# Kernel tuning notes

Measured on AMD Instinct MI355X. Metric: run time of the kernel, lower is better.

## Reference

```python
import jax, jax.numpy as jnp
import numpy as np

BLOCK = 32            # MX block size (base-class default)
FMT_MAX = 1.984375    # MXINT8 element max = 127/64 (concrete _quantize_elements choice)
QSTEP = 64.0          # quantization grid step 2^-6
BUDGET = 8.0          # cfg.msd_cycle_budget
THRESH = 0.0          # cfg.msd_budget_dynamic_threshold
ALPHA = 1.0           # cfg.msd_budget_dynamic_scale (mode='linear')
NEG = -60.0           # log2 sentinel for zero/negative values


def _safe_log2(x):
    return jnp.where(x > 0, jnp.log2(jnp.maximum(x, 1e-45)), NEG)


def _quantize_blocks(t):
    """Per-block shared fp32 scale + MXINT8-style element quantization.
    t: (rows, feat) with feat % BLOCK == 0 -> q (rows, nb, bs), scales (rows, nb)."""
    rows = t.shape[0]
    blocks = t.reshape(rows, -1, BLOCK)
    max_abs = jnp.max(jnp.abs(blocks), axis=-1)
    scales = jnp.maximum(max_abs / FMT_MAX, 1e-30)
    q = jnp.round(blocks / scales[..., None] * QSTEP) / QSTEP
    return q, scales


def _msd_truncate(value, num_digits):
    """Truncate each element to its num_digits most-significant NAF (BSD) digits."""
    abs_v = jnp.abs(value)
    sign = jnp.sign(value)
    mask = (num_digits > 0) & (abs_v > 0)
    msb_pos = jnp.floor(jnp.log2(jnp.maximum(abs_v, 1e-45)))
    scale_up = jnp.exp2(23.0 - msb_pos)              # place MSB at bit 23
    x_scaled = jnp.round(abs_v * scale_up).astype(jnp.int32)
    x_h = x_scaled >> 1
    s = x_scaled + x_h
    naf_pos = s & ~x_h
    naf_neg = x_h & ~s
    combined = naf_pos | naf_neg
    naf_width = jnp.where(
        combined > 0,
        jnp.floor(jnp.log2(jnp.maximum(combined.astype(jnp.float32), 1.0))).astype(jnp.int32) + 1,
        jnp.zeros_like(combined),
    )
    drop = jnp.clip(naf_width - num_digits.astype(jnp.int32), 0, 31)
    keep_mask = ~((jnp.int32(1) << drop) - 1)
    recon = ((naf_pos & keep_mask).astype(jnp.float32)
             - (naf_neg & keep_mask).astype(jnp.float32)) / scale_up
    return jnp.where(mask, sign * recon, jnp.zeros_like(recon))


def _forward(x, weight, bias):
    x_q, x_scales = _quantize_blocks(x)        # (N, nb, bs), (N, nb)
    w_q, w_scales = _quantize_blocks(weight)   # (O, nb, bs), (O, nb)
    # inter-block delays from shared scales
    combined_e = jnp.floor(_safe_log2(x_scales)[:, None, :]
                           + _safe_log2(w_scales)[None, :, :])   # (N, O, nb)
    e_max = jnp.max(combined_e, axis=-1)                         # (N, O)
    inter = e_max[..., None] - combined_e                        # (N, O, nb)
    # intra-block delays from activation element exponents
    abs_q = jnp.abs(x_q)
    elem_e = jnp.where(abs_q > 0, jnp.floor(jnp.log2(jnp.maximum(abs_q, 1e-45))), NEG)
    intra = jnp.max(elem_e, axis=-1, keepdims=True) - elem_e     # (N, nb, bs)
    # hybrid Glocal per-channel cycle budgets (linear dynamic mode)
    b_final = BUDGET + ALPHA * jnp.clip(e_max - THRESH, 0.0)     # (N, O)
    eff = (b_final[:, :, None, None]
           - inter[..., None]
           - intra[:, None, :, :])                               # (N, O, nb, bs)
    prod = x_q[:, None, :, :] * w_q[None, :, :, :]               # (N, O, nb, bs)
    trunc = jax.lax.stop_gradient(_msd_truncate(prod, eff))      # torch.no_grad()
    block_dot = jnp.sum(trunc, axis=-1)                          # (N, O, nb)
    out = jnp.einsum('nb,ob,nob->no', x_scales, w_scales, block_dot)
    return out + bias[None, :]


def setup_inputs() -> dict:
    key = jax.random.key(0)
    k1, k2, k3 = jax.random.split(key, 3)
    N, IN, OUT = 128, 1024, 512
    x = jax.random.normal(k1, (N, IN), dtype=jnp.float32)
    weight = jax.random.normal(k2, (OUT, IN), dtype=jnp.float32) * 0.02
    bias = jax.random.normal(k3, (OUT,), dtype=jnp.float32)
    return {"x": x, "weight": weight, "bias": bias}


def reference(x, weight, bias):
    return _forward(x, weight, bias)
```

## Files before the change

kernel.cpp:

```cpp
#include <hip/hip_runtime.h>
#include <math.h>

#define NROWS 128
#define KDIM  1024
#define ODIM  512
#define NB    32
#define BS    32

__device__ __forceinline__ int clz32(unsigned x) { return x ? __builtin_clz(x) : 32; }

__device__ __forceinline__ int naf_keep(int P, int isum, int allones) {
  int kept, h, t, c, dr;
  asm volatile(
      "v_ashrrev_i32 %1, 1, %5\n\t"
      "v_add_u32     %2, %5, %1\n\t"
      "v_xor_b32     %3, %2, %1\n\t"
      "v_ffbh_u32    %3, %3\n\t"
      "v_sub_u32     %4, %6, %3\n\t"
      "v_med3_i32    %4, %4, 0, 31\n\t"
      "v_lshlrev_b32 %3, %4, %7\n\t"
      "v_and_b32     %2, %2, %3\n\t"
      "v_and_b32     %1, %1, %3\n\t"
      "v_sub_u32     %0, %2, %1"
      : "=v"(kept), "=&v"(h), "=&v"(t), "=&v"(c), "=&v"(dr)
      : "v"(P), "v"(isum), "v"(allones));
  return kept;
}

__global__ __launch_bounds__(64)
void prep_kernel(const float* __restrict__ x, const float* __restrict__ wgt,
                 unsigned short* __restrict__ xp, unsigned char* __restrict__ wq,
                 float* __restrict__ xs, float* __restrict__ lxs,
                 float* __restrict__ wsc, float* __restrict__ lws) {
  __shared__ float sl[2112];
  const int b = blockIdx.x;
  const int lane = threadIdx.x;
  const bool isx = b < 64;
  const float* src = isx ? (x + (size_t)b * 2048)
                         : (wgt + (size_t)(b - 64) * 2048);
#pragma unroll
  for (int j = 0; j < 8; ++j) {
    float4 f = ((const float4*)src)[j * 64 + lane];
    int f0 = (j * 64 + lane) * 4;
    int s0 = f0 + (f0 >> 5);
    sl[s0] = f.x; sl[s0 + 1] = f.y; sl[s0 + 2] = f.z; sl[s0 + 3] = f.w;
  }
  __syncthreads();

  float v[32];
  float m = 0.f;
#pragma unroll
  for (int k = 0; k < 32; ++k) {
    v[k] = sl[lane * 33 + k];
    m = fmaxf(m, fabsf(v[k]));
  }
  const float scale = fmaxf(m / 1.984375f, 1e-30f);
  const int gt = (isx ? b : (b - 64)) * 64 + lane;
  const int row = gt >> 5, blk = gt & 31;

  if (isx) {
    int q[32], e[32], emax = -60;
#pragma unroll
    for (int i = 0; i < 32; ++i) {
      float t = v[i] / scale * 64.0f;
      int qi = (int)rintf(t);
      q[i] = qi;
      int a = qi < 0 ? -qi : qi;
      int ei = a ? (31 - clz32((unsigned)a)) - 6 : -60;
      e[i] = ei;
      emax = ei > emax ? ei : emax;
    }
    unsigned short u[32];
#pragma unroll
    for (int i = 0; i < 32; ++i)
      u[i] = (unsigned short)(((emax - e[i]) << 8) | (q[i] & 0xFF));
    uint4* dst = (uint4*)(xp + (size_t)row * KDIM + blk * BS);
#pragma unroll
    for (int i = 0; i < 4; ++i) {
      uint4 w4;
      w4.x = (unsigned)u[8*i+0] | ((unsigned)u[8*i+1] << 16);
      w4.y = (unsigned)u[8*i+2] | ((unsigned)u[8*i+3] << 16);
      w4.z = (unsigned)u[8*i+4] | ((unsigned)u[8*i+5] << 16);
      w4.w = (unsigned)u[8*i+6] | ((unsigned)u[8*i+7] << 16);
      dst[i] = w4;
    }
    xs[gt] = scale;
    lxs[gt] = (float)log2((double)scale);
  } else {
    unsigned char c[32];
#pragma unroll
    for (int i = 0; i < 32; ++i) {
      float t = v[i] / scale * 64.0f;
      int qi = (int)rintf(t);
      c[i] = (unsigned char)(qi & 0xFF);
    }
    uint4* dst = (uint4*)(wq + (size_t)row * KDIM + blk * BS);
#pragma unroll
    for (int i = 0; i < 2; ++i) {
      uint4 w4;
      w4.x = (unsigned)c[16*i+ 0] | ((unsigned)c[16*i+ 1] << 8) | ((unsigned)c[16*i+ 2] << 16) | ((unsigned)c[16*i+ 3] << 24);
      w4.y = (unsigned)c[16*i+ 4] | ((unsigned)c[16*i+ 5] << 8) | ((unsigned)c[16*i+ 6] << 16) | ((unsigned)c[16*i+ 7] << 24);
      w4.z = (unsigned)c[16*i+ 8] | ((unsigned)c[16*i+ 9] << 8) | ((unsigned)c[16*i+10] << 16) | ((unsigned)c[16*i+11] << 24);
      w4.w = (unsigned)c[16*i+12] | ((unsigned)c[16*i+13] << 8) | ((unsigned)c[16*i+14] << 16) | ((unsigned)c[16*i+15] << 24);
      dst[i] = w4;
    }
    wsc[gt] = scale;
    lws[gt] = (float)log2((double)scale);
  }
}

__global__ __launch_bounds__(1024, 8)
void msd_main_kernel(const unsigned short* __restrict__ xp,
                     const unsigned char* __restrict__ wq,
                     const float* __restrict__ xs, const float* __restrict__ lxs,
                     const float* __restrict__ wsc, const float* __restrict__ lws,
                     const float* __restrict__ bias, float* __restrict__ out) {
  __shared__ unsigned short sx[8][1032];
  __shared__ unsigned char  swq[16][1040];
  __shared__ float sxs[8][33], slx[8][33], sws[16][33], slw[16][33];
  __shared__ float sred[7 * 128];
  const int tid = threadIdx.x;
  const int n0 = blockIdx.x * 8, o0 = blockIdx.y * 16;

  {
    int r = tid >> 7, c = tid & 127;
    uint4 d = ((const uint4*)(xp + (size_t)(n0 + r) * KDIM))[c];
    *(uint4*)&sx[r][c * 8] = d;
  }
  {
    int r = tid >> 6, c = tid & 63;
    uint4 d = ((const uint4*)(wq + (size_t)(o0 + r) * KDIM))[c];
    *(uint4*)&swq[r][c * 16] = d;
  }
  {
    int r = tid >> 5, b = tid & 31;
    if (tid < 256) {
      sxs[r][b] = xs[(n0 + r) * NB + b];
      slx[r][b] = lxs[(n0 + r) * NB + b];
    }
    if (tid < 512) {
      sws[r][b] = wsc[(o0 + r) * NB + b];
      slw[r][b] = lws[(o0 + r) * NB + b];
    }
  }
  __syncthreads();

  const int kh = tid >> 7, idx = tid & 127, tn = idx >> 4, to = idx & 15;

  float emf = -1e30f;
#pragma unroll
  for (int b = 0; b < NB; ++b)
    emf = fmaxf(emf, floorf(slx[tn][b] + slw[to][b]));
  const int iemax = (int)emf;
  const int sbase = 24 + (iemax < 0 ? iemax : 0);

  const int allones = (int)0xFFFFFFFF;

  float facc = 0.f;
  const int b0 = kh * 4;
#pragma unroll 1
  for (int bb = 0; bb < 4; ++bb) {
    const int b = b0 + bb;
    const int ice = (int)floorf(slx[tn][b] + slw[to][b]);
    const int s = sbase - ice;
    uint4 xv0 = *(const uint4*)&sx[tn][b * 32 + 0];
    uint4 xv1 = *(const uint4*)&sx[tn][b * 32 + 8];
    uint4 xv2 = *(const uint4*)&sx[tn][b * 32 + 16];
    uint4 xv3 = *(const uint4*)&sx[tn][b * 32 + 24];
    unsigned xd[16] = {xv0.x, xv0.y, xv0.z, xv0.w, xv1.x, xv1.y, xv1.z, xv1.w,
                       xv2.x, xv2.y, xv2.z, xv2.w, xv3.x, xv3.y, xv3.z, xv3.w};
    uint4 wv0 = *(const uint4*)&swq[to][b * 32];
    uint4 wv1 = *(const uint4*)&swq[to][b * 32 + 16];
    unsigned wb[8] = {wv0.x, wv0.y, wv0.z, wv0.w, wv1.x, wv1.y, wv1.z, wv1.w};
    int bacc = 0;
#pragma unroll
    for (int j = 0; j < 16; ++j) {
      const unsigned xw = xd[j];
      const unsigned ww = wb[j >> 1];
      const int ix0 = __builtin_amdgcn_sbfe((int)xw, 0, 8);
      const int in0 = (int)__builtin_amdgcn_ubfe(xw, 8, 8);
      const int ix1 = __builtin_amdgcn_sbfe((int)xw, 16, 8);
      const int in1 = (int)(xw >> 24);
      int iw0, iw1;
      if (j & 1) { iw0 = __builtin_amdgcn_sbfe((int)ww, 16, 8);
                   iw1 = __builtin_amdgcn_sbfe((int)ww, 24, 8); }
      else       { iw0 = __builtin_amdgcn_sbfe((int)ww, 0, 8);
                   iw1 = __builtin_amdgcn_sbfe((int)ww, 8, 8); }
      bacc += naf_keep(__mul24(ix0, iw0), in0 + s, allones);
      bacc += naf_keep(__mul24(ix1, iw1), in1 + s, allones);
    }
    facc += sxs[tn][b] * sws[to][b] * (float)bacc;
  }

  if (kh) sred[(kh - 1) * 128 + idx] = facc;
  __syncthreads();
  if (!kh) {
    float r = facc;
#pragma unroll
    for (int p = 0; p < 7; ++p) r += sred[p * 128 + idx];
    r = r * (1.0f / 4096.0f) + bias[o0 + to];
    out[(size_t)(n0 + tn) * ODIM + (o0 + to)] = r;
  }
}

extern "C" void kernel_launch(void* const* d_in, const int* in_sizes, int n_in,
                              void* d_out, int out_size, void* d_ws, size_t ws_size,
                              hipStream_t stream) {
  const float* x    = (const float*)d_in[0];
  const float* wgt  = (const float*)d_in[1];
  const float* bias = (const float*)d_in[2];
  float* out = (float*)d_out;
  char* ws = (char*)d_ws;
  unsigned short* xp  = (unsigned short*)(ws + 0);
  unsigned char*  wq  = (unsigned char*)(ws + 262144);
  float* xs  = (float*)(ws + 786432);
  float* lxs = (float*)(ws + 802816);
  float* wsc = (float*)(ws + 819200);
  float* lws = (float*)(ws + 884736);

  hipLaunchKernelGGL(prep_kernel, dim3(320), dim3(64), 0, stream,
                     x, wgt, xp, wq, xs, lxs, wsc, lws);
  hipLaunchKernelGGL(msd_main_kernel, dim3(16, 32), dim3(1024), 0, stream,
                     xp, wq, xs, lxs, wsc, lws, bias, out);
}
```

Measured before the change: 35.63 us.

## Compute two outputs per thread, split K across 16 groups, precompute emax

Each thread now produces two output channels, sharing the x loads and field extraction between them, and the K dimension is split 16 ways of 2 blocks instead of 8 ways of 4. The per-(n,o) maximum combined exponent is computed once by 128 threads into shared memory rather than redundantly by all 1024 threads. The cost is an extra barrier, more register pressure, and a larger 15-way shared-memory reduction at the end.

```diff
diff --git a/kernel.cpp b/kernel.cpp
--- a/kernel.cpp
+++ b/kernel.cpp
@@ -118,7 +118,8 @@
   __shared__ unsigned short sx[8][1032];
   __shared__ unsigned char  swq[16][1040];
   __shared__ float sxs[8][33], slx[8][33], sws[16][33], slw[16][33];
-  __shared__ float sred[7 * 128];
+  __shared__ int   sE[8][17];
+  __shared__ float sred[15 * 128];
   const int tid = threadIdx.x;
   const int n0 = blockIdx.x * 8, o0 = blockIdx.y * 16;
 
@@ -145,61 +146,85 @@
   }
   __syncthreads();
 
-  const int kh = tid >> 7, idx = tid & 127, tn = idx >> 4, to = idx & 15;
-
-  float emf = -1e30f;
-#pragma unroll
-  for (int b = 0; b < NB; ++b)
-    emf = fmaxf(emf, floorf(slx[tn][b] + slw[to][b]));
-  const int iemax = (int)emf;
-  const int sbase = 24 + (iemax < 0 ? iemax : 0);
-
+  if (tid < 128) {
+    const int tn2 = tid >> 4, to2 = tid & 15;
+    float emf = -1e30f;
+#pragma unroll
+    for (int b = 0; b < NB; ++b)
+      emf = fmaxf(emf, floorf(slx[tn2][b] + slw[to2][b]));
+    const int iemax = (int)emf;
+    sE[tn2][to2] = 24 + (iemax < 0 ? iemax : 0);
+  }
+  __syncthreads();
+
+  const int kh = tid >> 6, idx = tid & 63, tn = idx >> 3, toa = idx & 7;
+  const int tob = toa + 8;
+  const int sbase_a = sE[tn][toa], sbase_b = sE[tn][tob];
   const int allones = (int)0xFFFFFFFF;
 
-  float facc = 0.f;
-  const int b0 = kh * 4;
-#pragma unroll 1
-  for (int bb = 0; bb < 4; ++bb) {
+  float facc_a = 0.f, facc_b = 0.f;
+  const int b0 = kh * 2;
+#pragma unroll
+  for (int bb = 0; bb < 2; ++bb) {
     const int b = b0 + bb;
-    const int ice = (int)floorf(slx[tn][b] + slw[to][b]);
-    const int s = sbase - ice;
-    uint4 xv0 = *(const uint4*)&sx[tn][b * 32 + 0];
-    uint4 xv1 = *(const uint4*)&sx[tn][b * 32 + 8];
-    uint4 xv2 = *(const uint4*)&sx[tn][b * 32 + 16];
-    uint4 xv3 = *(const uint4*)&sx[tn][b * 32 + 24];
-    unsigned xd[16] = {xv0.x, xv0.y, xv0.z, xv0.w, xv1.x, xv1.y, xv1.z, xv1.w,
-                       xv2.x, xv2.y, xv2.z, xv2.w, xv3.x, xv3.y, xv3.z, xv3.w};
-    uint4 wv0 = *(const uint4*)&swq[to][b * 32];
-    uint4 wv1 = *(const uint4*)&swq[to][b * 32 + 16];
-    unsigned wb[8] = {wv0.x, wv0.y, wv0.z, wv0.w, wv1.x, wv1.y, wv1.z, wv1.w};
-    int bacc = 0;
-#pragma unroll
-    for (int j = 0; j < 16; ++j) {
-      const unsigned xw = xd[j];
-      const unsigned ww = wb[j >> 1];
-      const int ix0 = __builtin_amdgcn_sbfe((int)xw, 0, 8);
-      const int in0 = (int)__builtin_amdgcn_ubfe(xw, 8, 8);
-      const int ix1 = __builtin_amdgcn_sbfe((int)xw, 16, 8);
-      const int in1 = (int)(xw >> 24);
-      int iw0, iw1;
-      if (j & 1) { iw0 = __builtin_amdgcn_sbfe((int)ww, 16, 8);
-                   iw1 = __builtin_amdgcn_sbfe((int)ww, 24, 8); }
-      else       { iw0 = __builtin_amdgcn_sbfe((int)ww, 0, 8);
-                   iw1 = __builtin_amdgcn_sbfe((int)ww, 8, 8); }
-      bacc += naf_keep(__mul24(ix0, iw0), in0 + s, allones);
-      bacc += naf_keep(__mul24(ix1, iw1), in1 + s, allones);
-    }
-    facc += sxs[tn][b] * sws[to][b] * (float)bacc;
-  }
-
-  if (kh) sred[(kh - 1) * 128 + idx] = facc;
+    const int s_a = sbase_a - (int)floorf(slx[tn][b] + slw[toa][b]);
+    const int s_b = sbase_b - (int)floorf(slx[tn][b] + slw[tob][b]);
+    const float cf_a = sxs[tn][b] * sws[toa][b];
+    const float cf_b = sxs[tn][b] * sws[tob][b];
+    int bacc_a = 0, bacc_b = 0;
+#pragma unroll
+    for (int hh = 0; hh < 2; ++hh) {
+      const uint4 xu0 = *(const uint4*)&sx[tn][b * 32 + hh * 16];
+      const uint4 xu1 = *(const uint4*)&sx[tn][b * 32 + hh * 16 + 8];
+      const uint4 wau = *(const uint4*)&swq[toa][b * 32 + hh * 16];
+      const uint4 wbu = *(const uint4*)&swq[tob][b * 32 + hh * 16];
+      const unsigned xw8[8] = {xu0.x, xu0.y, xu0.z, xu0.w,
+                               xu1.x, xu1.y, xu1.z, xu1.w};
+      const unsigned wa4[4] = {wau.x, wau.y, wau.z, wau.w};
+      const unsigned wb4[4] = {wbu.x, wbu.y, wbu.z, wbu.w};
+#pragma unroll
+      for (int j = 0; j < 8; ++j) {
+        const unsigned xw = xw8[j];
+        const unsigned wwa = wa4[j >> 1];
+        const unsigned wwb = wb4[j >> 1];
+        const int ix0 = __builtin_amdgcn_sbfe((int)xw, 0, 8);
+        const int in0 = (int)__builtin_amdgcn_ubfe(xw, 8, 8);
+        const int ix1 = __builtin_amdgcn_sbfe((int)xw, 16, 8);
+        const int in1 = (int)(xw >> 24);
+        int iwa0, iwa1, iwb0, iwb1;
+        if (j & 1) { iwa0 = __builtin_amdgcn_sbfe((int)wwa, 16, 8);
+                     iwa1 = __builtin_amdgcn_sbfe((int)wwa, 24, 8);
+                     iwb0 = __builtin_amdgcn_sbfe((int)wwb, 16, 8);
+                     iwb1 = __builtin_amdgcn_sbfe((int)wwb, 24, 8); }
+        else       { iwa0 = __builtin_amdgcn_sbfe((int)wwa, 0, 8);
+                     iwa1 = __builtin_amdgcn_sbfe((int)wwa, 8, 8);
+                     iwb0 = __builtin_amdgcn_sbfe((int)wwb, 0, 8);
+                     iwb1 = __builtin_amdgcn_sbfe((int)wwb, 8, 8); }
+        bacc_a += naf_keep(__mul24(ix0, iwa0), in0 + s_a, allones);
+        bacc_a += naf_keep(__mul24(ix1, iwa1), in1 + s_a, allones);
+        bacc_b += naf_keep(__mul24(ix0, iwb0), in0 + s_b, allones);
+        bacc_b += naf_keep(__mul24(ix1, iwb1), in1 + s_b, allones);
+      }
+    }
+    facc_a += cf_a * (float)bacc_a;
+    facc_b += cf_b * (float)bacc_b;
+  }
+
+  const int oa = tn * 16 + toa, ob = oa + 8;
+  if (kh) {
+    sred[(kh - 1) * 128 + oa] = facc_a;
+    sred[(kh - 1) * 128 + ob] = facc_b;
+  }
   __syncthreads();
   if (!kh) {
-    float r = facc;
-#pragma unroll
-    for (int p = 0; p < 7; ++p) r += sred[p * 128 + idx];
-    r = r * (1.0f / 4096.0f) + bias[o0 + to];
-    out[(size_t)(n0 + tn) * ODIM + (o0 + to)] = r;
+    float ra = facc_a, rb = facc_b;
+#pragma unroll
+    for (int p = 0; p < 15; ++p) {
+      ra += sred[p * 128 + oa];
+      rb += sred[p * 128 + ob];
+    }
+    out[(size_t)(n0 + tn) * ODIM + (o0 + toa)] = ra * (1.0f / 4096.0f) + bias[o0 + toa];
+    out[(size_t)(n0 + tn) * ODIM + (o0 + tob)] = rb * (1.0f / 4096.0f) + bias[o0 + tob];
   }
 }
 
```

After: 34.34 us. 1.04x faster.
